# Performance work log

Hardware: AMD Instinct MI355X
Metric: run time of the kernel (lower is better)

## Reference

```python
import jax, jax.numpy as jnp
import numpy as np

N = 40000      # input points
M = 40000      # output points
E = 500000     # flat neighbor edges (ragged flattened)
F = 32         # input feature channels
C = 64         # output channels
K = 15         # kernel points
EXTENT = 0.6


def _make_kernel_points(k, radius):
    # Deterministic stand-in for load_kernels(): first point fixed at center,
    # remaining points spread inside a ball of the given radius.
    rng = np.random.RandomState(0)
    pts = rng.randn(k, 3).astype(np.float32)
    pts /= np.linalg.norm(pts, axis=1, keepdims=True) + 1e-9
    scale = rng.rand(k, 1).astype(np.float32) ** (1.0 / 3.0)
    pts = pts * scale * radius
    pts[0] = 0.0  # fixed='center'
    return jnp.asarray(pts)


def setup_inputs() -> dict:
    key = jax.random.key(0)
    ks = jax.random.split(key, 6)
    points = jax.random.uniform(ks[0], (N, 3), dtype=jnp.float32)
    features = jax.random.normal(ks[1], (N, F), dtype=jnp.float32)
    output_points = jax.random.uniform(ks[2], (M, 3), dtype=jnp.float32)
    neighbor_indices = jax.random.randint(ks[3], (E,), 0, N, dtype=jnp.int32)
    segment_ids = jnp.sort(jax.random.randint(ks[4], (E,), 0, M, dtype=jnp.int32))
    k_points = _make_kernel_points(K, 1.5 * EXTENT)          # [K,3] constant
    k_values = jax.random.normal(ks[5], (K, F, C), dtype=jnp.float32) * 0.05
    return {
        "points": points,
        "features": features,
        "output_points": output_points,
        "neighbor_indices": neighbor_indices,
        "segment_ids": segment_ids,
        "k_points": k_points,
        "k_values": k_values,
    }


def reference(points, features, output_points, neighbor_indices, segment_ids,
              k_points, k_values):
    # Gather neighbor coords/features and recenter around each output point.
    rel = points[neighbor_indices] - output_points[segment_ids]      # [E,3]
    nbr_feat = features[neighbor_indices]                            # [E,F]

    # Per-kernel-point squared distances and linear influence weights.
    diff = rel[:, None, :] - k_points[None, :, :]                    # [E,K,3]
    sq_dist = jnp.sum(diff * diff, axis=-1)                          # [E,K]
    w = jnp.maximum(1.0 - jnp.sqrt(sq_dist) / EXTENT, 0.0)           # [E,K]

    # Weighted features and ragged segment-sum per output point.
    weighted = w[:, :, None] * nbr_feat[:, None, :]                  # [E,K,F]
    agg = jax.ops.segment_sum(weighted, segment_ids, num_segments=M,
                              indices_are_sorted=True)               # [M,K,F]

    # Batched matmul over kernel points, then sum over kernel points.
    out = jnp.einsum('mkf,kfc->mc', agg, k_values)                   # [M,C]
    return out
```

## Files before the change

### kernel.cpp

```cpp
#include <hip/hip_runtime.h>

typedef __attribute__((ext_vector_type(8))) short bf16x8;
typedef __attribute__((ext_vector_type(8))) _Float16 f16x8;
typedef __attribute__((ext_vector_type(4))) float f32x4;
typedef __attribute__((ext_vector_type(4))) _Float16 f16x4;
typedef __attribute__((ext_vector_type(2))) _Float16 f16x2;

#define NPTS   40000
#define MOUT   40000
#define EDG    500000
#define FIN    32
#define COUT   64
#define KP     15
#define KFDIM  (KP * FIN)
#define EXTENT 0.6f

#define FSTRIDE 112
#define WSTRIDE 40
#define WAVE_LDS (16 * FSTRIDE + 16 * WSTRIDE)
#define ASTR 488

#define FEAT_BLKS  (NPTS * FIN / 1024)
#define PTS_BLKS   ((NPTS + 255) / 256)
#define OP_BLKS    ((MOUT + 255) / 256)
#define ROW_BLKS   ((EDG + 255) / 256)
#define WT_BLKS    (KFDIM * COUT / 256)
#define PRE_BLKS   (FEAT_BLKS + PTS_BLKS + OP_BLKS + ROW_BLKS + WT_BLKS)

__device__ __forceinline__ short f2bf(float x) {
    union { float f; unsigned u; } v; v.f = x;
    unsigned r = (v.u + 0x7fffu + ((v.u >> 16) & 1u)) >> 16;
    return (short)r;
}

__global__ __launch_bounds__(256) void preprocess_all(
    const float* __restrict__ features, _Float16* __restrict__ feat_i,
    const float* __restrict__ pts, float4* __restrict__ p4,
    const float* __restrict__ opts, float4* __restrict__ op4,
    const int* __restrict__ seg_ids, int* __restrict__ row_start,
    const float* __restrict__ k_values, _Float16* __restrict__ w_t)
{
    const int bid = blockIdx.x;
    if (bid < FEAT_BLKS) {
        const int d0 = (bid * 256 + threadIdx.x) * 4;
        #pragma unroll
        for (int u = 0; u < 4; ++u) {
            const int d = d0 + u;
            const int p = d >> 5, q = d & 31;
            const int fp = q >> 1, h = q & 1;
            feat_i[d] = (_Float16)features[p * FIN + fp + 16 * h];
        }
    } else if (bid < FEAT_BLKS + PTS_BLKS) {
        const int i = (bid - FEAT_BLKS) * 256 + threadIdx.x;
        if (i < NPTS) {
            const float* p = pts + 3 * i;
            p4[i] = make_float4(p[0], p[1], p[2], 0.f);
        }
    } else if (bid < FEAT_BLKS + PTS_BLKS + OP_BLKS) {
        const int i = (bid - FEAT_BLKS - PTS_BLKS) * 256 + threadIdx.x;
        if (i < MOUT) {
            const float* p = opts + 3 * i;
            op4[i] = make_float4(p[0], p[1], p[2], 0.f);
        }
    } else if (bid < FEAT_BLKS + PTS_BLKS + OP_BLKS + ROW_BLKS) {
        const int e = (bid - FEAT_BLKS - PTS_BLKS - OP_BLKS) * 256 + threadIdx.x;
        if (e >= EDG) return;
        const int cur  = seg_ids[e];
        const int prev = (e == 0) ? -1 : seg_ids[e - 1];
        for (int m = prev + 1; m <= cur; ++m) row_start[m] = e;
        if (e == EDG - 1)
            for (int m = cur + 1; m <= MOUT; ++m) row_start[m] = EDG;
    } else {
        const int d = (bid - FEAT_BLKS - PTS_BLKS - OP_BLKS - ROW_BLKS) * 256
                      + threadIdx.x;
        const int c = d / KFDIM, r = d % KFDIM;
        const int k = r >> 5, q = r & 31;
        const int fp = q >> 1, h = q & 1;
        w_t[d] = (_Float16)k_values[(k * FIN + fp + 16 * h) * COUT + c];
    }
}

__global__ __launch_bounds__(256, 6) void kpconv_fused2(
    const float4* __restrict__ points4,
    const _Float16* __restrict__ feat_i,
    const float4* __restrict__ op4,
    const int*   __restrict__ nbr_idx,
    const int*   __restrict__ row_start,
    const float* __restrict__ k_points,
    const _Float16* __restrict__ w_t,
    float* __restrict__ out)
{
    __shared__ __align__(16) _Float16 aggT[16 * ASTR];
    __shared__ __align__(16) unsigned char stage[4 * WAVE_LDS];

    const int tid  = threadIdx.x;
    const int wave = tid >> 6;
    const int lane = tid & 63;
    const int quad = lane >> 4;
    const int l16  = lane & 15;
    const int esl  = lane >> 2;
    const int kg   = lane & 3;
    const int m0   = blockIdx.x * 16;

    unsigned char* fbase = stage + wave * WAVE_LDS;
    unsigned char* wbase = fbase + 16 * FSTRIDE;

    float kx[4], ky[4], kz[4];
    #pragma unroll
    for (int t = 0; t < 4; ++t) {
        const int k  = kg * 4 + t;
        const int kk = k < KP ? k : 0;
        kx[t] = k_points[kk * 3 + 0];
        ky[t] = k_points[kk * 3 + 1];
        kz[t] = k_points[kk * 3 + 2];
    }
    const float inv_ext = 1.f / EXTENT;

    for (int s4 = 0; s4 < 4; ++s4) {
        const int li = wave * 4 + s4;
        const int m  = m0 + li;
        const int e0 = row_start[m];
        const int e1 = row_start[m + 1];
        const float4 o = op4[m];

        f32x4 c_lo = {0.f, 0.f, 0.f, 0.f};
        f32x4 c_hi = {0.f, 0.f, 0.f, 0.f};

        for (int es = e0; es < e1; es += 16) {
            const int e  = es + esl;
            const int nb = nbr_idx[e < e1 ? e : e1 - 1];

            const uint4 fc = *(const uint4*)(feat_i + nb * FIN + kg * 8);
            *(uint4*)(fbase + esl * FSTRIDE + kg * 16) = fc;

            const float4 p = points4[nb];
            const float rx = p.x - o.x, ry = p.y - o.y, rz = p.z - o.z;
            const bool evalid = e < e1;
            #pragma unroll
            for (int t = 0; t < 4; ++t) {
                const float dx = rx - kx[t], dy = ry - ky[t], dz = rz - kz[t];
                float w = 1.f - sqrtf(dx * dx + dy * dy + dz * dz) * inv_ext;
                w = w > 0.f ? w : 0.f;
                if (!evalid || (kg * 4 + t) >= KP) w = 0.f;
                *(_Float16*)(wbase + (kg * 4 + t) * WSTRIDE + esl * 2) = (_Float16)w;
            }

            const f16x4 af = *(const f16x4*)(wbase + l16 * WSTRIDE + quad * 8);
            f16x2 w2[4];
            #pragma unroll
            for (int j = 0; j < 4; ++j)
                w2[j] = *(const f16x2*)(fbase + (quad * 4 + j) * FSTRIDE + l16 * 4);
            const f16x4 blo = {w2[0][0], w2[1][0], w2[2][0], w2[3][0]};
            const f16x4 bhi = {w2[0][1], w2[1][1], w2[2][1], w2[3][1]};

            c_lo = __builtin_amdgcn_mfma_f32_16x16x16f16(af, blo, c_lo, 0, 0, 0);
            c_hi = __builtin_amdgcn_mfma_f32_16x16x16f16(af, bhi, c_hi, 0, 0, 0);
        }

        _Float16* dst = aggT + li * ASTR;
        #pragma unroll
        for (int r = 0; r < 4; ++r) {
            const int krow = quad * 4 + r;
            if (krow < KP) {
                f16x2 v = {(_Float16)c_lo[r], (_Float16)c_hi[r]};
                *(f16x2*)(dst + krow * 32 + 2 * l16) = v;
            }
        }
    }

    __syncthreads();

    const int bcol = wave * 16 + l16;
    const _Float16* wrow = w_t + (size_t)bcol * KFDIM + quad * 8;
    const _Float16* arow = aggT + l16 * ASTR + quad * 8;

    f32x4 c = {0.f, 0.f, 0.f, 0.f};
    #pragma unroll
    for (int s = 0; s < 15; ++s) {
        const f16x8 a = *(const f16x8*)(arow + 32 * s);
        const f16x8 b = *(const f16x8*)(wrow + 32 * s);
        c = __builtin_amdgcn_mfma_f32_16x16x32_f16(a, b, c, 0, 0, 0);
    }

    #pragma unroll
    for (int r = 0; r < 4; ++r)
        out[(m0 + quad * 4 + r) * COUT + bcol] = c[r];
}

__global__ __launch_bounds__(256, 4) void kpconv_agg_fallback(
    const float* __restrict__ points,
    const float* __restrict__ features,
    const float* __restrict__ output_points,
    const int*   __restrict__ nbr_idx,
    const int*   __restrict__ seg_ids,
    const float* __restrict__ k_points,
    _Float16* __restrict__ agg_g)
{
    __shared__ int seg_start[5];

    const int tid = threadIdx.x;
    const int m0  = blockIdx.x * 4;

    if (tid <= 4) {
        const int target = m0 + tid;
        int lo = 0, hi = EDG;
        while (lo < hi) {
            int mid = (lo + hi) >> 1;
            if (seg_ids[mid] < target) lo = mid + 1; else hi = mid;
        }
        seg_start[tid] = lo;
    }
    __syncthreads();

    const int wave = tid >> 6;
    const int lane = tid & 63;
    const int quad = lane >> 4;
    const int l16  = lane & 15;

    const int m = m0 + wave;
    const float ox = output_points[m * 3 + 0];
    const float oy = output_points[m * 3 + 1];
    const float oz = output_points[m * 3 + 2];

    const int myk = l16 < KP ? l16 : 0;
    const float kpx = k_points[myk * 3 + 0];
    const float kpy = k_points[myk * 3 + 1];
    const float kpz = k_points[myk * 3 + 2];
    const float inv_ext = 1.f / EXTENT;

    const int e0 = seg_start[wave], e1 = seg_start[wave + 1];

    f32x4 c_lo = {0.f, 0.f, 0.f, 0.f};
    f32x4 c_hi = {0.f, 0.f, 0.f, 0.f};

    for (int es = e0; es < e1; es += 32) {
        const int last = e1 - 1;
        const int ebase = es + quad * 8;

        int nb[8];
        #pragma unroll
        for (int j = 0; j < 8; ++j) {
            const int e = ebase + j;
            nb[j] = nbr_idx[e < e1 ? e : last];
        }

        bf16x8 afrag, blo, bhi;
        #pragma unroll
        for (int j = 0; j < 8; ++j) {
            const float* pp = points + nb[j] * 3;
            const float rx = pp[0] - ox;
            const float ry = pp[1] - oy;
            const float rz = pp[2] - oz;
            const float dx = rx - kpx, dy = ry - kpy, dz = rz - kpz;
            const float d2 = dx * dx + dy * dy + dz * dz;
            float w = 1.f - sqrtf(d2) * inv_ext;
            w = w > 0.f ? w : 0.f;
            if (l16 >= KP || ebase + j >= e1) w = 0.f;
            afrag[j] = f2bf(w);
        }

        #pragma unroll
        for (int j = 0; j < 8; ++j) {
            const float* fp = features + nb[j] * FIN + l16;
            blo[j] = f2bf(fp[0]);
            bhi[j] = f2bf(fp[16]);
        }

        c_lo = __builtin_amdgcn_mfma_f32_16x16x32_bf16(afrag, blo, c_lo, 0, 0, 0);
        c_hi = __builtin_amdgcn_mfma_f32_16x16x32_bf16(afrag, bhi, c_hi, 0, 0, 0);
    }

    _Float16* dst = agg_g + (size_t)m * KFDIM;
    #pragma unroll
    for (int r = 0; r < 4; ++r) {
        const int krow = quad * 4 + r;
        if (krow < KP) {
            dst[krow * FIN + l16]      = (_Float16)c_lo[r];
            dst[krow * FIN + 16 + l16] = (_Float16)c_hi[r];
        }
    }
}

__global__ __launch_bounds__(256, 4) void kpconv_gemm_plain(
    const _Float16* __restrict__ agg_g,
    const float* __restrict__ k_values,
    float* __restrict__ out)
{
    const int tid  = threadIdx.x;
    const int wave = tid >> 6;
    const int lane = tid & 63;
    const int quad = lane >> 4;
    const int l16  = lane & 15;
    const int m0   = blockIdx.x * 32;
    const int bcol = wave * 16 + l16;

    f16x8 bfr[15];
    #pragma unroll
    for (int s = 0; s < 15; ++s) {
        #pragma unroll
        for (int j = 0; j < 8; ++j)
            bfr[s][j] = (_Float16)k_values[(32 * s + quad * 8 + j) * COUT + bcol];
    }

    const _Float16* arow0 = agg_g + (size_t)(m0 + l16) * KFDIM + quad * 8;
    const _Float16* arow1 = arow0 + 16 * KFDIM;

    f32x4 c0 = {0.f, 0.f, 0.f, 0.f};
    f32x4 c1 = {0.f, 0.f, 0.f, 0.f};
    #pragma unroll
    for (int s = 0; s < 15; ++s) {
        const f16x8 a0 = *(const f16x8*)(arow0 + 32 * s);
        const f16x8 a1 = *(const f16x8*)(arow1 + 32 * s);
        c0 = __builtin_amdgcn_mfma_f32_16x16x32_f16(a0, bfr[s], c0, 0, 0, 0);
        c1 = __builtin_amdgcn_mfma_f32_16x16x32_f16(a1, bfr[s], c1, 0, 0, 0);
    }

    #pragma unroll
    for (int r = 0; r < 4; ++r) {
        out[(m0 + quad * 4 + r) * COUT + bcol]      = c0[r];
        out[(m0 + 16 + quad * 4 + r) * COUT + bcol] = c1[r];
    }
}

extern "C" void kernel_launch(void* const* d_in, const int* in_sizes, int n_in,
                              void* d_out, int out_size, void* d_ws, size_t ws_size,
                              hipStream_t stream) {
    const float* points        = (const float*)d_in[0];
    const float* features      = (const float*)d_in[1];
    const float* output_points = (const float*)d_in[2];
    const int*   nbr_idx       = (const int*)d_in[3];
    const int*   seg_ids       = (const int*)d_in[4];
    const float* k_points      = (const float*)d_in[5];
    const float* k_values      = (const float*)d_in[6];
    float* out = (float*)d_out;

    const size_t feat_bytes = (size_t)NPTS * FIN * sizeof(_Float16);
    const size_t pts4_bytes = (size_t)NPTS * sizeof(float4);
    const size_t op4_bytes  = (size_t)MOUT * sizeof(float4);
    const size_t rs_bytes   = ((size_t)(MOUT + 1) * sizeof(int) + 15) & ~15ul;
    const size_t wt_bytes   = (size_t)KFDIM * COUT * sizeof(_Float16);
    const size_t full_bytes = feat_bytes + pts4_bytes + op4_bytes + rs_bytes
                            + wt_bytes;

    if (ws_size >= full_bytes) {
        char* p = (char*)d_ws;
        _Float16* feat_i    = (_Float16*)p;  p += feat_bytes;
        float4*   points4   = (float4*)p;    p += pts4_bytes;
        float4*   op4       = (float4*)p;    p += op4_bytes;
        int*      row_start = (int*)p;       p += rs_bytes;
        _Float16* w_t       = (_Float16*)p;

        preprocess_all<<<PRE_BLKS, 256, 0, stream>>>(
            features, feat_i, points, points4, output_points, op4,
            seg_ids, row_start, k_values, w_t);
        kpconv_fused2<<<MOUT / 16, 256, 0, stream>>>(
            points4, feat_i, op4, nbr_idx, row_start, k_points, w_t, out);
    } else {
        _Float16* agg_g = (_Float16*)d_ws;
        kpconv_agg_fallback<<<MOUT / 4, 256, 0, stream>>>(
            points, features, output_points, nbr_idx, seg_ids, k_points, agg_g);
        kpconv_gemm_plain<<<MOUT / 32, 256, 0, stream>>>(agg_g, k_values, out);
    }
}
```

Baseline: 107.9 us.

## Software-prefetch neighbor gathers across edge chunks and rows in aggregation loop

Each wave now loads its five row_start bounds up front and keeps a 64-entry window of neighbor indices in a register, fetching individual indices with lane shuffles instead of a global load per chunk. The feature and point gathers for the next 16-edge chunk, including the first chunk of the next non-empty row, are issued before the current chunk is processed, so gather latency overlaps the weight computation and MFMA work. The extra live registers for the prefetched data are covered by lowering the launch-bounds occupancy hint from 6 to 5 blocks per CU. That may reduce latency hiding from other waves.

Measured after the change: 101.9 us. 5.5% less time.

```diff
diff --git a/kernel.cpp b/kernel.cpp
--- a/kernel.cpp
+++ b/kernel.cpp
@@ -80,7 +80,7 @@
     }
 }
 
-__global__ __launch_bounds__(256, 6) void kpconv_fused2(
+__global__ __launch_bounds__(256, 5) void kpconv_fused2(
     const float4* __restrict__ points4,
     const _Float16* __restrict__ feat_i,
     const float4* __restrict__ op4,
@@ -116,26 +116,55 @@
     }
     const float inv_ext = 1.f / EXTENT;
 
-    for (int s4 = 0; s4 < 4; ++s4) {
-        const int li = wave * 4 + s4;
-        const int m  = m0 + li;
-        const int e0 = row_start[m];
-        const int e1 = row_start[m + 1];
-        const float4 o = op4[m];
+    int rs[5];
+    #pragma unroll
+    for (int i = 0; i < 5; ++i) rs[i] = row_start[m0 + wave * 4 + i];
+
+    int nstart[4];
+    nstart[3] = rs[4];
+    nstart[2] = (rs[3] < rs[4]) ? rs[3] : rs[4];
+    nstart[1] = (rs[2] < rs[3]) ? rs[2] : nstart[2];
+    nstart[0] = (rs[1] < rs[2]) ? rs[1] : nstart[1];
+    const int fstart = (rs[0] < rs[1]) ? rs[0] : nstart[0];
+
+    int wb = -0x40000000;
+    int nbrreg = 0;
+    uint4  fc_n = {0, 0, 0, 0};
+    float4 p_n  = make_float4(0.f, 0.f, 0.f, 0.f);
+
+    auto pref = [&](int es) {
+        if (es + 15 > wb + 63) {
+            wb = es;
+            const int a = wb + lane;
+            nbrreg = nbr_idx[a < EDG ? a : EDG - 1];
+        }
+        const int e  = es + esl;
+        const int nb = __shfl(nbrreg, e - wb);
+        fc_n = *(const uint4*)(feat_i + nb * FIN + kg * 8);
+        p_n  = ((const float4*)points4)[nb];
+    };
+
+    pref(fstart);
+
+    #pragma unroll
+    for (int j = 0; j < 4; ++j) {
+        const int e0 = rs[j];
+        const int e1 = rs[j + 1];
+        const float4 o = op4[m0 + wave * 4 + j];
 
         f32x4 c_lo = {0.f, 0.f, 0.f, 0.f};
         f32x4 c_hi = {0.f, 0.f, 0.f, 0.f};
 
         for (int es = e0; es < e1; es += 16) {
-            const int e  = es + esl;
-            const int nb = nbr_idx[e < e1 ? e : e1 - 1];
-
-            const uint4 fc = *(const uint4*)(feat_i + nb * FIN + kg * 8);
+            const uint4  fc = fc_n;
+            const float4 p  = p_n;
+            const int nes = (es + 16 < e1) ? es + 16 : nstart[j];
+            pref(nes);
+
             *(uint4*)(fbase + esl * FSTRIDE + kg * 16) = fc;
 
-            const float4 p = points4[nb];
             const float rx = p.x - o.x, ry = p.y - o.y, rz = p.z - o.z;
-            const bool evalid = e < e1;
+            const bool evalid = (es + esl) < e1;
             #pragma unroll
             for (int t = 0; t < 4; ++t) {
                 const float dx = rx - kx[t], dy = ry - ky[t], dz = rz - kz[t];
@@ -148,8 +177,8 @@
             const f16x4 af = *(const f16x4*)(wbase + l16 * WSTRIDE + quad * 8);
             f16x2 w2[4];
             #pragma unroll
-            for (int j = 0; j < 4; ++j)
-                w2[j] = *(const f16x2*)(fbase + (quad * 4 + j) * FSTRIDE + l16 * 4);
+            for (int jj = 0; jj < 4; ++jj)
+                w2[jj] = *(const f16x2*)(fbase + (quad * 4 + jj) * FSTRIDE + l16 * 4);
             const f16x4 blo = {w2[0][0], w2[1][0], w2[2][0], w2[3][0]};
             const f16x4 bhi = {w2[0][1], w2[1][1], w2[2][1], w2[3][1]};
 
@@ -157,7 +186,7 @@
             c_hi = __builtin_amdgcn_mfma_f32_16x16x16f16(af, bhi, c_hi, 0, 0, 0);
         }
 
-        _Float16* dst = aggT + li * ASTR;
+        _Float16* dst = aggT + (wave * 4 + j) * ASTR;
         #pragma unroll
         for (int r = 0; r < 4; ++r) {
             const int krow = quad * 4 + r;
```

## Register-pipeline edge gathers across segments, drop LDS staging in aggregation

Applied to the files above, without the earlier changes.

Replaces the per-output-point loop, which staged features and weights through LDS, with a flattened stream over all edges of a wave's four output points. Neighbor indices and point coordinates are loaded once per 64 edges and shared across lanes with shuffles, and feature loads are double-buffered in registers so the next tile's gathers overlap the current tile's weight computation and MFMAs. Each lane now computes weights for a single kernel point directly in MFMA A-operand layout, and empty rows are handled by zero-filling aggT up front. The change raises register pressure, so the occupancy hint drops from 6 to 4 blocks per CU, and the control flow for advancing across segments becomes more complex.

Measured after the change: 135.4 us. +25.5%, slower.

```diff
diff --git a/kernel.cpp b/kernel.cpp
--- a/kernel.cpp
+++ b/kernel.cpp
@@ -15,9 +15,6 @@
 #define KFDIM  (KP * FIN)
 #define EXTENT 0.6f
 
-#define FSTRIDE 112
-#define WSTRIDE 40
-#define WAVE_LDS (16 * FSTRIDE + 16 * WSTRIDE)
 #define ASTR 488
 
 #define FEAT_BLKS  (NPTS * FIN / 1024)
@@ -80,7 +77,7 @@
     }
 }
 
-__global__ __launch_bounds__(256, 6) void kpconv_fused2(
+__global__ __launch_bounds__(256, 4) void kpconv_fused2(
     const float4* __restrict__ points4,
     const _Float16* __restrict__ feat_i,
     const float4* __restrict__ op4,
@@ -91,82 +88,168 @@
     float* __restrict__ out)
 {
     __shared__ __align__(16) _Float16 aggT[16 * ASTR];
-    __shared__ __align__(16) unsigned char stage[4 * WAVE_LDS];
 
     const int tid  = threadIdx.x;
     const int wave = tid >> 6;
     const int lane = tid & 63;
     const int quad = lane >> 4;
     const int l16  = lane & 15;
-    const int esl  = lane >> 2;
-    const int kg   = lane & 3;
     const int m0   = blockIdx.x * 16;
 
-    unsigned char* fbase = stage + wave * WAVE_LDS;
-    unsigned char* wbase = fbase + 16 * FSTRIDE;
-
-    float kx[4], ky[4], kz[4];
-    #pragma unroll
-    for (int t = 0; t < 4; ++t) {
-        const int k  = kg * 4 + t;
-        const int kk = k < KP ? k : 0;
-        kx[t] = k_points[kk * 3 + 0];
-        ky[t] = k_points[kk * 3 + 1];
-        kz[t] = k_points[kk * 3 + 2];
-    }
+    {
+        char* z = (char*)(aggT + wave * 4 * ASTR);
+        #pragma unroll
+        for (int i = 0; i < 4; ++i) {
+            const int c = i * 64 + lane;
+            if (c < 244) *(uint4*)(z + c * 16) = make_uint4(0, 0, 0, 0);
+        }
+    }
+
+    const int  myk = l16 < KP ? l16 : 0;
+    const float kxx = k_points[myk * 3 + 0];
+    const float kyy = k_points[myk * 3 + 1];
+    const float kzz = k_points[myk * 3 + 2];
+    const bool  vk  = (l16 < KP);
     const float inv_ext = 1.f / EXTENT;
 
-    for (int s4 = 0; s4 < 4; ++s4) {
-        const int li = wave * 4 + s4;
-        const int m  = m0 + li;
-        const int e0 = row_start[m];
-        const int e1 = row_start[m + 1];
-        const float4 o = op4[m];
-
-        f32x4 c_lo = {0.f, 0.f, 0.f, 0.f};
-        f32x4 c_hi = {0.f, 0.f, 0.f, 0.f};
-
-        for (int es = e0; es < e1; es += 16) {
-            const int e  = es + esl;
-            const int nb = nbr_idx[e < e1 ? e : e1 - 1];
-
-            const uint4 fc = *(const uint4*)(feat_i + nb * FIN + kg * 8);
-            *(uint4*)(fbase + esl * FSTRIDE + kg * 16) = fc;
-
-            const float4 p = points4[nb];
-            const float rx = p.x - o.x, ry = p.y - o.y, rz = p.z - o.z;
-            const bool evalid = e < e1;
-            #pragma unroll
-            for (int t = 0; t < 4; ++t) {
-                const float dx = rx - kx[t], dy = ry - ky[t], dz = rz - kz[t];
-                float w = 1.f - sqrtf(dx * dx + dy * dy + dz * dz) * inv_ext;
-                w = w > 0.f ? w : 0.f;
-                if (!evalid || (kg * 4 + t) >= KP) w = 0.f;
-                *(_Float16*)(wbase + (kg * 4 + t) * WSTRIDE + esl * 2) = (_Float16)w;
-            }
-
-            const f16x4 af = *(const f16x4*)(wbase + l16 * WSTRIDE + quad * 8);
-            f16x2 w2[4];
-            #pragma unroll
-            for (int j = 0; j < 4; ++j)
-                w2[j] = *(const f16x2*)(fbase + (quad * 4 + j) * FSTRIDE + l16 * 4);
-            const f16x4 blo = {w2[0][0], w2[1][0], w2[2][0], w2[3][0]};
-            const f16x4 bhi = {w2[0][1], w2[1][1], w2[2][1], w2[3][1]};
-
-            c_lo = __builtin_amdgcn_mfma_f32_16x16x16f16(af, blo, c_lo, 0, 0, 0);
-            c_hi = __builtin_amdgcn_mfma_f32_16x16x16f16(af, bhi, c_hi, 0, 0, 0);
-        }
-
-        _Float16* dst = aggT + li * ASTR;
-        #pragma unroll
-        for (int r = 0; r < 4; ++r) {
-            const int krow = quad * 4 + r;
-            if (krow < KP) {
-                f16x2 v = {(_Float16)c_lo[r], (_Float16)c_hi[r]};
-                *(f16x2*)(dst + krow * 32 + 2 * l16) = v;
-            }
-        }
-    }
+    int rs[5];
+    #pragma unroll
+    for (int i = 0; i < 5; ++i) rs[i] = row_start[m0 + wave * 4 + i];
+
+    const float4 o0 = op4[m0 + wave * 4 + 0];
+    const float4 o1 = op4[m0 + wave * 4 + 1];
+    const float4 o2 = op4[m0 + wave * 4 + 2];
+    const float4 o3 = op4[m0 + wave * 4 + 3];
+
+    int n3es = rs[4], n3e1 = rs[4], n3j = 4;
+    int n2es, n2e1, n2j;
+    if (rs[3] < rs[4]) { n2es = rs[3]; n2e1 = rs[4]; n2j = 3; }
+    else               { n2es = n3es;  n2e1 = n3e1;  n2j = n3j; }
+    int n1es, n1e1, n1j;
+    if (rs[2] < rs[3]) { n1es = rs[2]; n1e1 = rs[3]; n1j = 2; }
+    else               { n1es = n2es;  n1e1 = n2e1;  n1j = n2j; }
+    int n0es, n0e1, n0j;
+    if (rs[1] < rs[2]) { n0es = rs[1]; n0e1 = rs[2]; n0j = 1; }
+    else               { n0es = n1es;  n0e1 = n1e1;  n0j = n1j; }
+
+    int esA, e1A, jA;
+    if (rs[0] < rs[1]) { esA = rs[0]; e1A = rs[1]; jA = 0; }
+    else               { esA = n0es;  e1A = n0e1;  jA = n0j; }
+
+    auto adv = [&](int es, int e1, int j, int& res, int& re1, int& rj) {
+        const int nes_ = (j == 0) ? n0es : (j == 1) ? n1es : (j == 2) ? n2es : n3es;
+        const int ne1_ = (j == 0) ? n0e1 : (j == 1) ? n1e1 : (j == 2) ? n2e1 : n3e1;
+        const int nj_  = (j == 0) ? n0j  : (j == 1) ? n1j  : (j == 2) ? n2j  : n3j;
+        const bool more = (es + 16 < e1);
+        res = more ? es + 16 : nes_;
+        re1 = more ? e1 : ne1_;
+        rj  = more ? j : nj_;
+    };
+
+    int wb = -0x40000000;
+    int nbrreg = 0;
+    float pwx = 0.f, pwy = 0.f, pwz = 0.f;
+    float pxb[2][4], pyb[2][4], pzb[2][4];
+    unsigned ftb[2][4];
+
+#define PREF(B, ES)                                                           \
+    {                                                                         \
+        const int es_ = (ES);                                                 \
+        if (es_ + 15 > wb + 63) {                                             \
+            wb = es_;                                                         \
+            const int a_  = wb + lane;                                        \
+            const int ac_ = a_ < EDG ? a_ : EDG - 1;                          \
+            nbrreg = nbr_idx[ac_];                                            \
+            const float4 pw_ = points4[nbrreg];                               \
+            pwx = pw_.x; pwy = pw_.y; pwz = pw_.z;                            \
+        }                                                                     \
+        const int base_ = es_ - wb + quad * 4;                                \
+        _Pragma("unroll")                                                     \
+        for (int jj = 0; jj < 4; ++jj) {                                      \
+            const int nb_ = __shfl(nbrreg, base_ + jj);                       \
+            ftb[B][jj] = *(const unsigned*)(feat_i + nb_ * FIN + 2 * l16);    \
+            pxb[B][jj] = __shfl(pwx, base_ + jj);                             \
+            pyb[B][jj] = __shfl(pwy, base_ + jj);                             \
+            pzb[B][jj] = __shfl(pwz, base_ + jj);                             \
+        }                                                                     \
+    }
+
+#define FLUSH()                                                               \
+    if (cur_j >= 0) {                                                         \
+        _Float16* dst_ = aggT + (wave * 4 + cur_j) * ASTR;                    \
+        _Pragma("unroll")                                                     \
+        for (int r = 0; r < 4; ++r) {                                         \
+            const int krow_ = quad * 4 + r;                                   \
+            if (krow_ < KP) {                                                 \
+                f16x2 v_ = {(_Float16)c_lo[r], (_Float16)c_hi[r]};            \
+                *(f16x2*)(dst_ + krow_ * 32 + 2 * l16) = v_;                  \
+            }                                                                 \
+        }                                                                     \
+        c_lo = (f32x4){0.f, 0.f, 0.f, 0.f};                                   \
+        c_hi = (f32x4){0.f, 0.f, 0.f, 0.f};                                   \
+    }
+
+#define SELECT_O()                                                            \
+    {                                                                         \
+        ox = cur_j == 0 ? o0.x : cur_j == 1 ? o1.x : cur_j == 2 ? o2.x : o3.x;\
+        oy = cur_j == 0 ? o0.y : cur_j == 1 ? o1.y : cur_j == 2 ? o2.y : o3.y;\
+        oz = cur_j == 0 ? o0.z : cur_j == 1 ? o1.z : cur_j == 2 ? o2.z : o3.z;\
+    }
+
+#define CONSUME(B, ES, E1, J)                                                 \
+    {                                                                         \
+        if ((J) != cur_j) { FLUSH(); cur_j = (J); SELECT_O(); }               \
+        f16x4 af;                                                             \
+        _Pragma("unroll")                                                     \
+        for (int jj = 0; jj < 4; ++jj) {                                      \
+            const float rx_ = pxb[B][jj] - ox;                                \
+            const float ry_ = pyb[B][jj] - oy;                                \
+            const float rz_ = pzb[B][jj] - oz;                                \
+            const float dx_ = rx_ - kxx, dy_ = ry_ - kyy, dz_ = rz_ - kzz;    \
+            float w_ = 1.f - sqrtf(dx_*dx_ + dy_*dy_ + dz_*dz_) * inv_ext;    \
+            w_ = w_ > 0.f ? w_ : 0.f;                                         \
+            if (!vk || ((ES) + quad * 4 + jj) >= (E1)) w_ = 0.f;              \
+            af[jj] = (_Float16)w_;                                            \
+        }                                                                     \
+        union { unsigned u; f16x2 h; } u0_, u1_, u2_, u3_;                    \
+        u0_.u = ftb[B][0]; u1_.u = ftb[B][1];                                 \
+        u2_.u = ftb[B][2]; u3_.u = ftb[B][3];                                 \
+        const f16x4 blo_ = {u0_.h[0], u1_.h[0], u2_.h[0], u3_.h[0]};          \
+        const f16x4 bhi_ = {u0_.h[1], u1_.h[1], u2_.h[1], u3_.h[1]};          \
+        c_lo = __builtin_amdgcn_mfma_f32_16x16x16f16(af, blo_, c_lo, 0, 0, 0);\
+        c_hi = __builtin_amdgcn_mfma_f32_16x16x16f16(af, bhi_, c_hi, 0, 0, 0);\
+    }
+
+    int cur_j = -1;
+    float ox = 0.f, oy = 0.f, oz = 0.f;
+    f32x4 c_lo = {0.f, 0.f, 0.f, 0.f};
+    f32x4 c_hi = {0.f, 0.f, 0.f, 0.f};
+
+    int esB, e1B, jB;
+    adv(esA, e1A, jA, esB, e1B, jB);
+    PREF(0, esA)
+    PREF(1, esB)
+
+    for (;;) {
+        if (esA >= e1A) break;
+        int esC, e1C, jC;
+        adv(esB, e1B, jB, esC, e1C, jC);
+        CONSUME(0, esA, e1A, jA)
+        PREF(0, esC)
+        if (esB >= e1B) break;
+        int esD, e1D, jD;
+        adv(esC, e1C, jC, esD, e1D, jD);
+        CONSUME(1, esB, e1B, jB)
+        PREF(1, esD)
+        esA = esC; e1A = e1C; jA = jC;
+        esB = esD; e1B = e1D; jB = jD;
+    }
+    FLUSH()
+
+#undef PREF
+#undef FLUSH
+#undef SELECT_O
+#undef CONSUME
 
     __syncthreads();
 
```
